# Kernel tuning notes

Hardware: AMD Instinct MI355X
Metric: run time of the kernel (lower is better)

The kernel has to match this reference:

```python
import jax, jax.numpy as jnp
import numpy as np
from jax import lax

B, S, M, D, NQ = 128, 100, 50, 128, 10000


def _xavier(key, shape):
    fan_in, fan_out = shape[0], shape[-1]
    limit = float(np.sqrt(6.0 / (fan_in + fan_out)))
    return jax.random.uniform(key, shape, jnp.float32, -limit, limit)


def setup_inputs() -> dict:
    key = jax.random.key(0)
    ks = jax.random.split(key, 16)
    return {
        "question_seq": jax.random.randint(ks[0], (B, S), 0, NQ),
        "answer_seq": jax.random.randint(ks[1], (B, S), 0, 2),
        "emb": _xavier(ks[2], (NQ, D)),
        "key_matrix": _xavier(ks[3], (M, D)),
        "vu_w1": _xavier(ks[4], (2 * D, D)),
        "vu_b1": jnp.zeros((D,), jnp.float32),
        "vu_w2": _xavier(ks[5], (D, D)),
        "vu_b2": jnp.zeros((D,), jnp.float32),
        "er_w": _xavier(ks[6], (D, D)),
        "er_b": jnp.zeros((D,), jnp.float32),
        "ad_w": _xavier(ks[7], (D, D)),
        "ad_b": jnp.zeros((D,), jnp.float32),
        "out_w1": _xavier(ks[8], (2 * D, D)),
        "out_b1": jnp.zeros((D,), jnp.float32),
        "out_w2": _xavier(ks[9], (D, 1)),
        "out_b2": jnp.zeros((1,), jnp.float32),
    }


def reference(question_seq, answer_seq, emb, key_matrix,
              vu_w1, vu_b1, vu_w2, vu_b2,
              er_w, er_b, ad_w, ad_b,
              out_w1, out_b1, out_w2, out_b2):
    # q_embed for all steps: [B,S,D]; attention over memory slots: [B,S,M]
    q_emb = emb[question_seq]
    attn = jax.nn.softmax(jnp.einsum('bsd,md->bsm', q_emb, key_matrix), axis=-1)

    def step(v, inp):
        w, qe = inp                                   # w: [B,M], qe: [B,D]
        read = jnp.einsum('bm,bmd->bd', w, v)         # attention read
        u = jnp.concatenate([read, qe], axis=-1)      # [B,2D]
        h = jnp.tanh(u @ vu_w1 + vu_b1)
        up = h @ vu_w2 + vu_b2                        # update vector [B,D]
        e = jax.nn.sigmoid(up @ er_w + er_b)          # erase gate
        a = jnp.tanh(up @ ad_w + ad_b)                # add vector
        v = v * (1.0 - w[:, :, None] * e[:, None, :]) + w[:, :, None] * a[:, None, :]
        return v, None

    v0 = jnp.zeros((B, M, D), q_emb.dtype)
    vT, _ = lax.scan(step, v0, (attn.transpose(1, 0, 2), q_emb.transpose(1, 0, 2)))

    # predict with last question (target_question=None branch)
    last_qe = q_emb[:, -1]                            # [B,D]
    last_w = attn[:, -1]                              # [B,M]
    read = jnp.einsum('bm,bmd->bd', last_w, vT)
    p_in = jnp.concatenate([read, last_qe], axis=-1)
    h = jax.nn.relu(p_in @ out_w1 + out_b1)
    pred = jax.nn.sigmoid(h @ out_w2 + out_b2)[:, 0]  # [B]
    return pred
```

## Files before the change

### kernel.cpp

```cpp
#include <hip/hip_runtime.h>

#define BB 128
#define SS 100
#define MM 50
#define DD 128
#define KROW 66
#define XW(k) ((k) + 8 * ((k) >> 5))
#define DUPW(k) ((k) + 8 * ((k) >> 5))

typedef float f32x2 __attribute__((ext_vector_type(2)));

#if defined(__has_builtin)
#  if __has_builtin(__builtin_elementwise_fma)
#    define HAVE_PKFMA 1
#  endif
#  if __has_builtin(__builtin_amdgcn_update_dpp)
#    define HAVE_DPP 1
#  endif
#endif

__device__ __forceinline__ f32x2 pkfma(f32x2 a, f32x2 b, f32x2 c) {
#ifdef HAVE_PKFMA
    return __builtin_elementwise_fma(a, b, c);
#else
    f32x2 r; r.x = fmaf(a.x, b.x, c.x); r.y = fmaf(a.y, b.y, c.y); return r;
#endif
}

__device__ __forceinline__ float qbf_add(float x) {
#ifdef HAVE_DPP
    union { float f; int i; } c, o;
    c.f = x;
    o.i = __builtin_amdgcn_update_dpp(0, c.i, 0xB1, 0xF, 0xF, true);
    x += o.f;
    c.f = x;
    o.i = __builtin_amdgcn_update_dpp(0, c.i, 0x4E, 0xF, 0xF, true);
    return x + o.f;
#else
    x += __shfl_xor(x, 1);
    x += __shfl_xor(x, 2);
    return x;
#endif
}

__device__ __forceinline__ float bf2f(unsigned short u) {
    union { unsigned int i; float f; } c; c.i = ((unsigned int)u) << 16; return c.f;
}
__device__ __forceinline__ float bfu_lo(unsigned int u) {
    union { unsigned int i; float f; } c; c.i = u << 16; return c.f;
}
__device__ __forceinline__ float bfu_hi(unsigned int u) {
    union { unsigned int i; float f; } c; c.i = u & 0xffff0000u; return c.f;
}
__device__ __forceinline__ unsigned short f2bf_bits(float f) {
    union { float f; unsigned int u; } c; c.f = f;
    unsigned int r = (c.u + 0x7FFFu + ((c.u >> 16) & 1u)) >> 16;
    return (unsigned short)r;
}
__device__ __forceinline__ unsigned int packbf(float lo, float hi) {
    return (unsigned int)f2bf_bits(lo) | ((unsigned int)f2bf_bits(hi) << 16);
}
__device__ __forceinline__ float fast_sigmoid(float x) { return 1.0f / (1.0f + __expf(-x)); }
__device__ __forceinline__ float fast_tanh(float x) {
    float ax = fabsf(x);
    float z = __expf(-2.0f * ax);
    float r = (1.0f - z) / (1.0f + z);
    return copysignf(r, x);
}

template <bool BF16>
__device__ __forceinline__ float ldw(const void* p, size_t idx) {
    if (BF16) return bf2f(((const unsigned short*)p)[idx]);
    return ((const float*)p)[idx];
}

#define W2ROW(r) ((r) * 68 + (((r) >> 5) << 3))

struct __align__(16) SmemT {
    union {
        struct {
            unsigned int key_w[MM * KROW];
            unsigned int qe8[8][68];
        } pre;
        struct {
            float xread[152];
            float xhdup[312];
            float h1f[DD];
        } run;
    } u;
    union {
        unsigned int w2s[8724];
        struct {
            unsigned int wrow_p[SS][32];
            unsigned short qp_all[SS][DD];
        } tab;
    } v2;
    int qrow[SS];
    float qlast[DD];
};

template <bool BF16>
__device__ void dkvmn_impl(
    const int* __restrict__ qseq,
    const void* emb, const void* key,
    const void* vu_w1, const void* vu_b1, const void* vu_w2, const void* vu_b2,
    const void* er_w, const void* er_b, const void* ad_w, const void* ad_b,
    const void* out_w1, const void* out_b1, const void* out_w2, const void* out_b2,
    void* outp, SmemT& sm)
{
    const int t = threadIdx.x;
    const int b = blockIdx.x;
    const int l = t & 63;
    const int wv = t >> 6;
    const int q = l & 3;
    const int d = (wv << 4) + (l >> 2);

    if (BF16) {
        const unsigned int* kg = (const unsigned int*)key;
        for (int g = t; g < MM * 64; g += 512)
            sm.u.pre.key_w[(g >> 6) * KROW + (g & 63)] = kg[g];
        const unsigned int* wg = (const unsigned int*)vu_w2;
        for (int g = t; g < 128 * 64; g += 512)
            sm.v2.w2s[W2ROW(g >> 6) + (g & 63)] = wg[g];
    } else {
        const float* kf = (const float*)key;
        for (int g = t; g < MM * 64; g += 512) {
            int row = g >> 6, c2 = g & 63;
            sm.u.pre.key_w[row * KROW + c2] = packbf(kf[row * 128 + 2 * c2], kf[row * 128 + 2 * c2 + 1]);
        }
        const float* wf = (const float*)vu_w2;
        for (int g = t; g < 128 * 64; g += 512) {
            int row = g >> 6, c2 = g & 63;
            sm.v2.w2s[W2ROW(row) + c2] = packbf(wf[row * 128 + 2 * c2], wf[row * 128 + 2 * c2 + 1]);
        }
    }
    for (int g = t; g < SS; g += 512) sm.qrow[g] = qseq[b * SS + g];
    __syncthreads();

    f32x2 rw2ea[32];
#pragma unroll
    for (int k = 0; k < 32; ++k) { rw2ea[k].x = 0.f; rw2ea[k].y = 0.f; }
    f32x2 eab2; eab2.x = 0.f; eab2.y = 0.f;
#pragma unroll 1
    for (int jc = 0; jc < 4; ++jc) {
        f32x2 ea[32];
#pragma unroll
        for (int i = 0; i < 32; ++i) {
            int j = 32 * jc + i;
            ea[i].x = ldw<BF16>(er_w, (size_t)j * DD + d);
            ea[i].y = ldw<BF16>(ad_w, (size_t)j * DD + d);
            float b2j = ldw<BF16>(vu_b2, j);
            f32x2 bs; bs.x = b2j; bs.y = b2j;
            eab2 = pkfma(bs, ea[i], eab2);
        }
#pragma unroll
        for (int k = 0; k < 32; ++k) {
            const uint4* wp = (const uint4*)&sm.v2.w2s[W2ROW(32 * q + k) + 16 * jc];
            uint4 A = wp[0], B = wp[1], C = wp[2], Dv = wp[3];
            unsigned int W[16] = { A.x, A.y, A.z, A.w, B.x, B.y, B.z, B.w,
                                   C.x, C.y, C.z, C.w, Dv.x, Dv.y, Dv.z, Dv.w };
            f32x2 acc = rw2ea[k];
#pragma unroll
            for (int wd = 0; wd < 16; ++wd) {
                float wlo = bfu_lo(W[wd]), whi = bfu_hi(W[wd]);
                f32x2 s0; s0.x = wlo; s0.y = wlo;
                f32x2 s1; s1.x = whi; s1.y = whi;
                acc = pkfma(s0, ea[2 * wd], acc);
                acc = pkfma(s1, ea[2 * wd + 1], acc);
            }
            rw2ea[k] = acc;
        }
    }
    eab2.x += ldw<BF16>(er_b, d);
    eab2.y += ldw<BF16>(ad_b, d);
    __syncthreads();

    f32x2 rw1a2[16];
    float rw1b[32];
#pragma unroll
    for (int i = 0; i < 16; ++i) {
        int k0 = 32 * q + 2 * i;
        rw1a2[i].x = ldw<BF16>(vu_w1, (size_t)k0 * DD + d);
        rw1a2[i].y = ldw<BF16>(vu_w1, (size_t)(k0 + 1) * DD + d);
    }
#pragma unroll
    for (int i = 0; i < 32; ++i)
        rw1b[i] = ldw<BF16>(vu_w1, (size_t)(DD + 32 * q + i) * DD + d);
    const float b1r = ldw<BF16>(vu_b1, d);

    for (int ii = 0; ii < 13; ++ii) {
        const int nrows = (ii == 12) ? 4 : 8;
        {
            int r = t >> 6, w = t & 63;
            if (r < nrows) {
                int row = sm.qrow[8 * ii + r];
                if (BF16) {
                    sm.u.pre.qe8[r][w] = ((const unsigned int*)emb)[((size_t)row << 6) + w];
                } else {
                    const float* ef = (const float*)emb + (((size_t)row) << 7) + 2 * w;
                    sm.u.pre.qe8[r][w] = packbf(ef[0], ef[1]);
                }
            }
        }
        __syncthreads();

        if (wv < nrows) {
            int m = l;
            int mc = (m < MM) ? m : (MM - 1);
            float a0 = 0.f, a1 = 0.f, a2 = 0.f, a3 = 0.f;
#pragma unroll
            for (int j = 0; j < 32; ++j) {
                uint2 kw = *(const uint2*)&sm.u.pre.key_w[mc * KROW + 2 * j];
                uint2 qw = *(const uint2*)&sm.u.pre.qe8[wv][2 * j];
                a0 = fmaf(bfu_lo(kw.x), bfu_lo(qw.x), a0);
                a1 = fmaf(bfu_hi(kw.x), bfu_hi(qw.x), a1);
                a2 = fmaf(bfu_lo(kw.y), bfu_lo(qw.y), a2);
                a3 = fmaf(bfu_hi(kw.y), bfu_hi(qw.y), a3);
            }
            float lg = (a0 + a1) + (a2 + a3);
            if (m >= MM) lg = -1e30f;
            float mx = lg;
#pragma unroll
            for (int o = 32; o > 0; o >>= 1) mx = fmaxf(mx, __shfl_xor(mx, o));
            float p = (m < MM) ? __expf(lg - mx) : 0.f;
            float sum = p;
#pragma unroll
            for (int o = 32; o > 0; o >>= 1) sum += __shfl_xor(sum, o);
            p = p / sum;
            float pn = __shfl_xor(p, 4);
            if ((m & 4) == 0)
                sm.v2.tab.wrow_p[8 * ii + wv][(m & 3) * 8 + (m >> 3)] = packbf(p, pn);
        }

        for (int sr = 0; sr < nrows; ++sr) {
            float p0 = 0.f, p1 = 0.f;
#pragma unroll
            for (int i = 0; i < 16; ++i) {
                unsigned int uw = sm.u.pre.qe8[sr][16 * q + i];
                p0 = fmaf(rw1b[2 * i],     bfu_lo(uw), p0);
                p1 = fmaf(rw1b[2 * i + 1], bfu_hi(uw), p1);
            }
            float qpv = qbf_add(p0 + p1);
            if (q == 0) sm.v2.tab.qp_all[8 * ii + sr][d] = f2bf_bits(qpv);
        }
        __syncthreads();
    }

    if (t < 64) {
        unsigned int uw = sm.u.pre.qe8[3][t];
        sm.qlast[2 * t]     = bfu_lo(uw);
        sm.qlast[2 * t + 1] = bfu_hi(uw);
    }
    f32x2 v2[7];
#pragma unroll
    for (int p = 0; p < 7; ++p) { v2[p].x = 0.f; v2[p].y = 0.f; }
    f32x2 wr2[7];
    {
        const uint4* wp = (const uint4*)&sm.v2.tab.wrow_p[0][q * 8];
        uint4 w0 = wp[0], w1 = wp[1];
        unsigned int ww[8] = { w0.x, w0.y, w0.z, w0.w, w1.x, w1.y, w1.z, w1.w };
#pragma unroll
        for (int p = 0; p < 7; ++p) { wr2[p].x = bfu_lo(ww[p]); wr2[p].y = bfu_hi(ww[p]); }
    }
    if (t < 152) sm.u.run.xread[t] = 0.f;
    __syncthreads();

    for (int s = 0; s < SS; ++s) {
        {
            float qpv = bf2f(sm.v2.tab.qp_all[s][d]);
            const float4* xp = (const float4*)&sm.u.run.xread[40 * q];
            f32x2 acc2; acc2.x = 0.f; acc2.y = 0.f;
#pragma unroll
            for (int j = 0; j < 8; ++j) {
                float4 X = xp[j];
                f32x2 x01; x01.x = X.x; x01.y = X.y;
                f32x2 x23; x23.x = X.z; x23.y = X.w;
                acc2 = pkfma(rw1a2[2 * j], x01, acc2);
                acc2 = pkfma(rw1a2[2 * j + 1], x23, acc2);
            }
            float acc = qbf_add(acc2.x + acc2.y);
            float hh = fast_tanh(acc + qpv + b1r);
            if (q == 0) {
                f32x2 hd; hd.x = hh; hd.y = hh;
                *(f32x2*)&sm.u.run.xhdup[DUPW(2 * d)] = hd;
            }
        }
        __syncthreads();

        {
            f32x2 acc2; acc2.x = 0.f; acc2.y = 0.f;
#pragma unroll
            for (int blk = 0; blk < 2; ++blk) {
                const float4* xp = (const float4*)&sm.u.run.xhdup[80 * q + 40 * blk];
#pragma unroll
                for (int j = 0; j < 8; ++j) {
                    float4 X = xp[j];
                    f32x2 s0; s0.x = X.x; s0.y = X.y;
                    f32x2 s1; s1.x = X.z; s1.y = X.w;
                    int k = 16 * blk + 2 * j;
                    acc2 = pkfma(rw2ea[k], s0, acc2);
                    acc2 = pkfma(rw2ea[k + 1], s1, acc2);
                }
            }
            float ae = qbf_add(acc2.x);
            float aa = qbf_add(acc2.y);
            float e = fast_sigmoid(ae + eab2.x);
            float a = fast_tanh(aa + eab2.y);
            f32x2 me; me.x = -e; me.y = -e;
            f32x2 av; av.x = a;  av.y = a;
#pragma unroll
            for (int p = 0; p < 7; ++p)
                v2[p] = pkfma(wr2[p], pkfma(me, v2[p], av), v2[p]);
            if (s + 1 < SS) {
                const uint4* wp = (const uint4*)&sm.v2.tab.wrow_p[s + 1][q * 8];
                uint4 w0 = wp[0], w1 = wp[1];
                unsigned int ww[8] = { w0.x, w0.y, w0.z, w0.w, w1.x, w1.y, w1.z, w1.w };
#pragma unroll
                for (int p = 0; p < 7; ++p) { wr2[p].x = bfu_lo(ww[p]); wr2[p].y = bfu_hi(ww[p]); }
            }
            f32x2 racc; racc.x = 0.f; racc.y = 0.f;
#pragma unroll
            for (int p = 0; p < 7; ++p)
                racc = pkfma(wr2[p], v2[p], racc);
            float rr = qbf_add(racc.x + racc.y);
            if (q == 0) sm.u.run.xread[XW(d)] = rr;
        }
        __syncthreads();
    }

    float acc = 0.f;
    {
        const float4* xp = (const float4*)&sm.u.run.xread[40 * q];
        const float4* qp4 = (const float4*)&sm.qlast[32 * q];
#pragma unroll
        for (int j = 0; j < 8; ++j) {
            float4 xv = xp[j];
            float4 qv = qp4[j];
            int k = 32 * q + 4 * j;
            acc = fmaf(ldw<BF16>(out_w1, (size_t)k * DD + d),       xv.x, acc);
            acc = fmaf(ldw<BF16>(out_w1, (size_t)(k + 1) * DD + d), xv.y, acc);
            acc = fmaf(ldw<BF16>(out_w1, (size_t)(k + 2) * DD + d), xv.z, acc);
            acc = fmaf(ldw<BF16>(out_w1, (size_t)(k + 3) * DD + d), xv.w, acc);
            acc = fmaf(ldw<BF16>(out_w1, (size_t)(DD + k) * DD + d),     qv.x, acc);
            acc = fmaf(ldw<BF16>(out_w1, (size_t)(DD + k + 1) * DD + d), qv.y, acc);
            acc = fmaf(ldw<BF16>(out_w1, (size_t)(DD + k + 2) * DD + d), qv.z, acc);
            acc = fmaf(ldw<BF16>(out_w1, (size_t)(DD + k + 3) * DD + d), qv.w, acc);
        }
    }
    acc = qbf_add(acc);
    float h1 = fmaxf(acc + ldw<BF16>(out_b1, d), 0.f);
    if (q == 0) sm.u.run.h1f[d] = h1;
    __syncthreads();

    if (t < 64) {
        float xs = fmaf(sm.u.run.h1f[t], ldw<BF16>(out_w2, t),
                        sm.u.run.h1f[64 + t] * ldw<BF16>(out_w2, 64 + t));
#pragma unroll
        for (int o = 32; o > 0; o >>= 1) xs += __shfl_xor(xs, o);
        if (t == 0) {
            float pred = fast_sigmoid(xs + ldw<BF16>(out_b2, 0));
            if (BF16) ((unsigned short*)outp)[b] = f2bf_bits(pred);
            else      ((float*)outp)[b] = pred;
        }
    }
}

__global__ __launch_bounds__(512) void DKVMN_78546361909953_kernel(
    const int* __restrict__ qseq,
    const void* emb, const void* key,
    const void* vu_w1, const void* vu_b1, const void* vu_w2, const void* vu_b2,
    const void* er_w, const void* er_b, const void* ad_w, const void* ad_b,
    const void* out_w1, const void* out_b1, const void* out_w2, const void* out_b2,
    void* outp)
{
    __shared__ SmemT sm;

    const unsigned int* eu = (const unsigned int*)emb;
    int cnt = 0;
    for (int i = 0; i < 32; ++i) {
        unsigned int e8 = (eu[i] >> 7) & 0xFFu;
        cnt += (e8 >= 100u && e8 <= 127u) ? 1 : 0;
    }
    if (cnt >= 16)
        dkvmn_impl<true>(qseq, emb, key, vu_w1, vu_b1, vu_w2, vu_b2,
                         er_w, er_b, ad_w, ad_b, out_w1, out_b1, out_w2, out_b2, outp, sm);
    else
        dkvmn_impl<false>(qseq, emb, key, vu_w1, vu_b1, vu_w2, vu_b2,
                          er_w, er_b, ad_w, ad_b, out_w1, out_b1, out_w2, out_b2, outp, sm);
}

extern "C" void kernel_launch(void* const* d_in, const int* in_sizes, int n_in,
                              void* d_out, int out_size, void* d_ws, size_t ws_size,
                              hipStream_t stream) {
    const int* qseq = (const int*)d_in[0];
    DKVMN_78546361909953_kernel<<<BB, 512, 0, stream>>>(
        qseq,
        d_in[2], d_in[3], d_in[4], d_in[5], d_in[6], d_in[7],
        d_in[8], d_in[9], d_in[10], d_in[11],
        d_in[12], d_in[13], d_in[14], d_in[15],
        d_out);
}
```

Measured before the change: 282.4 us.

## Split precompute and recurrent scan into two kernels via workspace

Splits the monolithic kernel into a precompute kernel and a scan kernel. The precompute kernel runs attention softmax, the question projection and the folded W2·[er,ad] matrix across 257 blocks, with each batch split into two halves of the sequence, and writes the results to a global workspace. The scan kernel then reads these, prefetching the next step's attention row and projection from global memory during the current step. The aim is to take the serial per-block prologue off the critical path and spread it over more CUs. The cost is an extra launch and the workspace traffic. A monolithic fallback remains for when the workspace is too small.

```diff
diff --git a/kernel.cpp b/kernel.cpp
--- a/kernel.cpp
+++ b/kernel.cpp
@@ -5,8 +5,6 @@
 #define MM 50
 #define DD 128
 #define KROW 66
-#define XW(k) ((k) + 8 * ((k) >> 5))
-#define DUPW(k) ((k) + 8 * ((k) >> 5))
 
 typedef float f32x2 __attribute__((ext_vector_type(2)));
 
@@ -74,9 +72,413 @@
     return ((const float*)p)[idx];
 }
 
+__device__ __forceinline__ bool detect_bf16(const void* emb) {
+    const unsigned int* eu = (const unsigned int*)emb;
+    int cnt = 0;
+    for (int i = 0; i < 32; ++i) {
+        unsigned int e8 = (eu[i] >> 7) & 0xFFu;
+        cnt += (e8 >= 100u && e8 <= 127u) ? 1 : 0;
+    }
+    return cnt >= 16;
+}
+
 #define W2ROW(r) ((r) * 68 + (((r) >> 5) << 3))
 
-struct __align__(16) SmemT {
+#define WS_WROW_OFF 0u
+#define WS_QP_OFF   (BB * SS * 32u * 4u)
+#define WS_W2EA_OFF (WS_QP_OFF + BB * SS * DD * 2u)
+#define WS_EAB_OFF  (WS_W2EA_OFF + DD * DD * 8u)
+#define WS_NEED     (WS_EAB_OFF + DD * 8u)
+
+struct __align__(16) SmemA {
+    union {
+        struct {
+            unsigned int key_w[MM * KROW];
+            unsigned int qe8[8][68];
+        } pre;
+        unsigned int w2s[8724];
+    } u;
+};
+
+template <bool BF16>
+__device__ void pre_impl(const int* qseq, const void* emb, const void* key,
+                         const void* vu_w1, unsigned int* wrow_g, unsigned short* qp_g,
+                         SmemA& sm)
+{
+    const int t = threadIdx.x;
+    const int b = blockIdx.x;
+    const int half = blockIdx.y;
+    const int l = t & 63;
+    const int wv = t >> 6;
+    const int q = l & 3;
+    const int d = (wv << 4) + (l >> 2);
+
+    if (BF16) {
+        const unsigned int* kg = (const unsigned int*)key;
+        for (int g = t; g < MM * 64; g += 512)
+            sm.u.pre.key_w[(g >> 6) * KROW + (g & 63)] = kg[g];
+    } else {
+        const float* kf = (const float*)key;
+        for (int g = t; g < MM * 64; g += 512) {
+            int row = g >> 6, c2 = g & 63;
+            sm.u.pre.key_w[row * KROW + c2] = packbf(kf[row * 128 + 2 * c2], kf[row * 128 + 2 * c2 + 1]);
+        }
+    }
+
+    float rw1b[32];
+#pragma unroll
+    for (int i = 0; i < 32; ++i)
+        rw1b[i] = ldw<BF16>(vu_w1, (size_t)(DD + 32 * q + i) * DD + d);
+    __syncthreads();
+
+    for (int ii = 0; ii < 7; ++ii) {
+        const int nrows = (ii == 6) ? 2 : 8;
+        {
+            int r = t >> 6, w = t & 63;
+            if (r < nrows) {
+                int s = 50 * half + 8 * ii + r;
+                int row = qseq[b * SS + s];
+                if (BF16) {
+                    sm.u.pre.qe8[r][w] = ((const unsigned int*)emb)[((size_t)row << 6) + w];
+                } else {
+                    const float* ef = (const float*)emb + (((size_t)row) << 7) + 2 * w;
+                    sm.u.pre.qe8[r][w] = packbf(ef[0], ef[1]);
+                }
+            }
+        }
+        __syncthreads();
+
+        if (wv < nrows) {
+            int m = l;
+            int mc = (m < MM) ? m : (MM - 1);
+            float a0 = 0.f, a1 = 0.f, a2 = 0.f, a3 = 0.f;
+#pragma unroll
+            for (int j = 0; j < 32; ++j) {
+                uint2 kw = *(const uint2*)&sm.u.pre.key_w[mc * KROW + 2 * j];
+                uint2 qw = *(const uint2*)&sm.u.pre.qe8[wv][2 * j];
+                a0 = fmaf(bfu_lo(kw.x), bfu_lo(qw.x), a0);
+                a1 = fmaf(bfu_hi(kw.x), bfu_hi(qw.x), a1);
+                a2 = fmaf(bfu_lo(kw.y), bfu_lo(qw.y), a2);
+                a3 = fmaf(bfu_hi(kw.y), bfu_hi(qw.y), a3);
+            }
+            float lg = (a0 + a1) + (a2 + a3);
+            if (m >= MM) lg = -1e30f;
+            float mx = lg;
+#pragma unroll
+            for (int o = 32; o > 0; o >>= 1) mx = fmaxf(mx, __shfl_xor(mx, o));
+            float p = (m < MM) ? __expf(lg - mx) : 0.f;
+            float sum = p;
+#pragma unroll
+            for (int o = 32; o > 0; o >>= 1) sum += __shfl_xor(sum, o);
+            p = p / sum;
+            float pn = __shfl_xor(p, 4);
+            int s = 50 * half + 8 * ii + wv;
+            if ((m & 4) == 0)
+                wrow_g[(size_t)(b * SS + s) * 32 + (m & 3) * 8 + (m >> 3)] = packbf(p, pn);
+        }
+
+        for (int sr = 0; sr < nrows; ++sr) {
+            float p0 = 0.f, p1 = 0.f;
+#pragma unroll
+            for (int i = 0; i < 16; ++i) {
+                unsigned int uw = sm.u.pre.qe8[sr][16 * q + i];
+                p0 = fmaf(rw1b[2 * i],     bfu_lo(uw), p0);
+                p1 = fmaf(rw1b[2 * i + 1], bfu_hi(uw), p1);
+            }
+            float qpv = qbf_add(p0 + p1);
+            int s = 50 * half + 8 * ii + sr;
+            if (q == 0) qp_g[(size_t)(b * SS + s) * DD + d] = f2bf_bits(qpv);
+        }
+        __syncthreads();
+    }
+}
+
+template <bool BF16>
+__device__ void build_impl(const void* vu_w2, const void* vu_b2,
+                           const void* er_w, const void* er_b,
+                           const void* ad_w, const void* ad_b,
+                           f32x2* w2ea_g, f32x2* eab_g, SmemA& sm)
+{
+    const int t = threadIdx.x;
+    const int l = t & 63;
+    const int wv = t >> 6;
+    const int q = l & 3;
+    const int d = (wv << 4) + (l >> 2);
+
+    if (BF16) {
+        const unsigned int* wg = (const unsigned int*)vu_w2;
+        for (int g = t; g < 128 * 64; g += 512)
+            sm.u.w2s[W2ROW(g >> 6) + (g & 63)] = wg[g];
+    } else {
+        const float* wf = (const float*)vu_w2;
+        for (int g = t; g < 128 * 64; g += 512) {
+            int row = g >> 6, c2 = g & 63;
+            sm.u.w2s[W2ROW(row) + c2] = packbf(wf[row * 128 + 2 * c2], wf[row * 128 + 2 * c2 + 1]);
+        }
+    }
+    __syncthreads();
+
+    f32x2 rw2ea[32];
+#pragma unroll
+    for (int k = 0; k < 32; ++k) { rw2ea[k].x = 0.f; rw2ea[k].y = 0.f; }
+    f32x2 eab2; eab2.x = 0.f; eab2.y = 0.f;
+#pragma unroll 1
+    for (int jc = 0; jc < 4; ++jc) {
+        f32x2 ea[32];
+#pragma unroll
+        for (int i = 0; i < 32; ++i) {
+            int j = 32 * jc + i;
+            ea[i].x = ldw<BF16>(er_w, (size_t)j * DD + d);
+            ea[i].y = ldw<BF16>(ad_w, (size_t)j * DD + d);
+            float b2j = ldw<BF16>(vu_b2, j);
+            f32x2 bs; bs.x = b2j; bs.y = b2j;
+            eab2 = pkfma(bs, ea[i], eab2);
+        }
+#pragma unroll
+        for (int k = 0; k < 32; ++k) {
+            const uint4* wp = (const uint4*)&sm.u.w2s[W2ROW(32 * q + k) + 16 * jc];
+            uint4 A = wp[0], B = wp[1], C = wp[2], Dv = wp[3];
+            unsigned int W[16] = { A.x, A.y, A.z, A.w, B.x, B.y, B.z, B.w,
+                                   C.x, C.y, C.z, C.w, Dv.x, Dv.y, Dv.z, Dv.w };
+            f32x2 acc = rw2ea[k];
+#pragma unroll
+            for (int wd = 0; wd < 16; ++wd) {
+                float wlo = bfu_lo(W[wd]), whi = bfu_hi(W[wd]);
+                f32x2 s0; s0.x = wlo; s0.y = wlo;
+                f32x2 s1; s1.x = whi; s1.y = whi;
+                acc = pkfma(s0, ea[2 * wd], acc);
+                acc = pkfma(s1, ea[2 * wd + 1], acc);
+            }
+            rw2ea[k] = acc;
+        }
+    }
+    eab2.x += ldw<BF16>(er_b, d);
+    eab2.y += ldw<BF16>(ad_b, d);
+
+#pragma unroll
+    for (int k = 0; k < 32; ++k)
+        w2ea_g[(size_t)(32 * q + k) * DD + d] = rw2ea[k];
+    if (q == 0) eab_g[d] = eab2;
+}
+
+__global__ __launch_bounds__(512) void DKVMN_78546361909953_pre(
+    const int* __restrict__ qseq,
+    const void* emb, const void* key, const void* vu_w1,
+    const void* vu_w2, const void* vu_b2,
+    const void* er_w, const void* er_b, const void* ad_w, const void* ad_b,
+    void* ws)
+{
+    __shared__ SmemA sm;
+    unsigned int*   wrow_g = (unsigned int*)((char*)ws + WS_WROW_OFF);
+    unsigned short* qp_g   = (unsigned short*)((char*)ws + WS_QP_OFF);
+    f32x2*          w2ea_g = (f32x2*)((char*)ws + WS_W2EA_OFF);
+    f32x2*          eab_g  = (f32x2*)((char*)ws + WS_EAB_OFF);
+    bool isbf = detect_bf16(emb);
+    if (blockIdx.x < BB) {
+        if (isbf) pre_impl<true>(qseq, emb, key, vu_w1, wrow_g, qp_g, sm);
+        else      pre_impl<false>(qseq, emb, key, vu_w1, wrow_g, qp_g, sm);
+    } else if (blockIdx.y == 0) {
+        if (isbf) build_impl<true>(vu_w2, vu_b2, er_w, er_b, ad_w, ad_b, w2ea_g, eab_g, sm);
+        else      build_impl<false>(vu_w2, vu_b2, er_w, er_b, ad_w, ad_b, w2ea_g, eab_g, sm);
+    }
+}
+
+struct __align__(16) SmemB {
+    float xread[152];
+    float xhdup[312];
+    float h1f[DD];
+    float qlast[DD];
+};
+
+template <bool BF16>
+__device__ void scan_impl(
+    const int* __restrict__ qseq,
+    const void* emb, const void* vu_w1, const void* vu_b1,
+    const void* out_w1, const void* out_b1, const void* out_w2, const void* out_b2,
+    const unsigned int* wrow_g, const unsigned short* qp_g,
+    const f32x2* w2ea_g, const f32x2* eab_g,
+    void* outp, SmemB& sm)
+{
+    const int t = threadIdx.x;
+    const int b = blockIdx.x;
+    const int l = t & 63;
+    const int q = l & 3;
+    const int d = ((t >> 6) << 4) + (l >> 2);
+
+    if (t < 64) {
+        int row = qseq[b * SS + (SS - 1)];
+        if (BF16) {
+            unsigned int uw = ((const unsigned int*)emb)[((size_t)row << 6) + t];
+            sm.qlast[2 * t]     = bfu_lo(uw);
+            sm.qlast[2 * t + 1] = bfu_hi(uw);
+        } else {
+            const float* ef = (const float*)emb + (((size_t)row) << 7) + 2 * t;
+            sm.qlast[2 * t]     = ef[0];
+            sm.qlast[2 * t + 1] = ef[1];
+        }
+    }
+
+    f32x2 rw1a2[16];
+#pragma unroll
+    for (int i = 0; i < 16; ++i) {
+        int k0 = 32 * q + 2 * i;
+        rw1a2[i].x = ldw<BF16>(vu_w1, (size_t)k0 * DD + d);
+        rw1a2[i].y = ldw<BF16>(vu_w1, (size_t)(k0 + 1) * DD + d);
+    }
+    const float b1r = ldw<BF16>(vu_b1, d);
+
+    f32x2 rw2ea[32];
+#pragma unroll
+    for (int k = 0; k < 32; ++k)
+        rw2ea[k] = w2ea_g[(size_t)(32 * q + k) * DD + d];
+    const f32x2 eab2 = eab_g[d];
+
+    f32x2 v2[7];
+#pragma unroll
+    for (int p = 0; p < 7; ++p) { v2[p].x = 0.f; v2[p].y = 0.f; }
+    f32x2 wr2[7];
+    {
+        const size_t r0 = (size_t)(b * SS) * 32 + q * 8;
+        uint4 w0 = *(const uint4*)&wrow_g[r0];
+        uint4 w1 = *(const uint4*)&wrow_g[r0 + 4];
+        unsigned int ww[8] = { w0.x, w0.y, w0.z, w0.w, w1.x, w1.y, w1.z, w1.w };
+#pragma unroll
+        for (int p = 0; p < 7; ++p) { wr2[p].x = bfu_lo(ww[p]); wr2[p].y = bfu_hi(ww[p]); }
+    }
+    unsigned short qpcur = qp_g[(size_t)(b * SS) * DD + d];
+
+    if (t < 152) sm.xread[t] = 0.f;
+    __syncthreads();
+
+    for (int s = 0; s < SS; ++s) {
+        uint4 pwA, pwB;
+        unsigned short pq = 0;
+        const bool hasnext = (s + 1 < SS);
+        if (hasnext) {
+            size_t r1 = (size_t)(b * SS + s + 1);
+            pwA = *(const uint4*)&wrow_g[r1 * 32 + q * 8];
+            pwB = *(const uint4*)&wrow_g[r1 * 32 + q * 8 + 4];
+            pq  = qp_g[r1 * DD + d];
+        }
+
+        {
+            float qpv = bf2f(qpcur);
+            const float4* xp = (const float4*)&sm.xread[40 * q];
+            f32x2 acc2; acc2.x = 0.f; acc2.y = 0.f;
+#pragma unroll
+            for (int j = 0; j < 8; ++j) {
+                float4 X = xp[j];
+                f32x2 x01; x01.x = X.x; x01.y = X.y;
+                f32x2 x23; x23.x = X.z; x23.y = X.w;
+                acc2 = pkfma(rw1a2[2 * j], x01, acc2);
+                acc2 = pkfma(rw1a2[2 * j + 1], x23, acc2);
+            }
+            float acc = qbf_add(acc2.x + acc2.y);
+            float hh = fast_tanh(acc + qpv + b1r);
+            if (q == 0) {
+                f32x2 hd; hd.x = hh; hd.y = hh;
+                *(f32x2*)&sm.xhdup[2 * d + 8 * ((2 * d) >> 5)] = hd;
+            }
+        }
+        __syncthreads();
+
+        {
+            f32x2 acc2; acc2.x = 0.f; acc2.y = 0.f;
+#pragma unroll
+            for (int blk = 0; blk < 2; ++blk) {
+                const float4* xp = (const float4*)&sm.xhdup[80 * q + 40 * blk];
+#pragma unroll
+                for (int j = 0; j < 8; ++j) {
+                    float4 X = xp[j];
+                    f32x2 s0; s0.x = X.x; s0.y = X.y;
+                    f32x2 s1; s1.x = X.z; s1.y = X.w;
+                    int k = 16 * blk + 2 * j;
+                    acc2 = pkfma(rw2ea[k], s0, acc2);
+                    acc2 = pkfma(rw2ea[k + 1], s1, acc2);
+                }
+            }
+            float ae = qbf_add(acc2.x);
+            float aa = qbf_add(acc2.y);
+            float e = fast_sigmoid(ae + eab2.x);
+            float a = fast_tanh(aa + eab2.y);
+            f32x2 me; me.x = -e; me.y = -e;
+            f32x2 av; av.x = a;  av.y = a;
+#pragma unroll
+            for (int p = 0; p < 7; ++p)
+                v2[p] = pkfma(wr2[p], pkfma(me, v2[p], av), v2[p]);
+            if (hasnext) {
+                unsigned int ww[8] = { pwA.x, pwA.y, pwA.z, pwA.w, pwB.x, pwB.y, pwB.z, pwB.w };
+#pragma unroll
+                for (int p = 0; p < 7; ++p) { wr2[p].x = bfu_lo(ww[p]); wr2[p].y = bfu_hi(ww[p]); }
+                qpcur = pq;
+            }
+            f32x2 racc; racc.x = 0.f; racc.y = 0.f;
+#pragma unroll
+            for (int p = 0; p < 7; ++p)
+                racc = pkfma(wr2[p], v2[p], racc);
+            float rr = qbf_add(racc.x + racc.y);
+            if (q == 0) sm.xread[rr == rr ? (d + 8 * (d >> 5)) : 0] = rr;
+        }
+        __syncthreads();
+    }
+
+    float acc = 0.f;
+    {
+        const float4* xp = (const float4*)&sm.xread[40 * q];
+        const float4* qp4 = (const float4*)&sm.qlast[32 * q];
+#pragma unroll
+        for (int j = 0; j < 8; ++j) {
+            float4 xv = xp[j];
+            float4 qv = qp4[j];
+            int k = 32 * q + 4 * j;
+            acc = fmaf(ldw<BF16>(out_w1, (size_t)k * DD + d),       xv.x, acc);
+            acc = fmaf(ldw<BF16>(out_w1, (size_t)(k + 1) * DD + d), xv.y, acc);
+            acc = fmaf(ldw<BF16>(out_w1, (size_t)(k + 2) * DD + d), xv.z, acc);
+            acc = fmaf(ldw<BF16>(out_w1, (size_t)(k + 3) * DD + d), xv.w, acc);
+            acc = fmaf(ldw<BF16>(out_w1, (size_t)(DD + k) * DD + d),     qv.x, acc);
+            acc = fmaf(ldw<BF16>(out_w1, (size_t)(DD + k + 1) * DD + d), qv.y, acc);
+            acc = fmaf(ldw<BF16>(out_w1, (size_t)(DD + k + 2) * DD + d), qv.z, acc);
+            acc = fmaf(ldw<BF16>(out_w1, (size_t)(DD + k + 3) * DD + d), qv.w, acc);
+        }
+    }
+    acc = qbf_add(acc);
+    float h1 = fmaxf(acc + ldw<BF16>(out_b1, d), 0.f);
+    if (q == 0) sm.h1f[d] = h1;
+    __syncthreads();
+
+    if (t < 64) {
+        float xs = fmaf(sm.h1f[t], ldw<BF16>(out_w2, t),
+                        sm.h1f[64 + t] * ldw<BF16>(out_w2, 64 + t));
+#pragma unroll
+        for (int o = 32; o > 0; o >>= 1) xs += __shfl_xor(xs, o);
+        if (t == 0) {
+            float pred = fast_sigmoid(xs + ldw<BF16>(out_b2, 0));
+            if (BF16) ((unsigned short*)outp)[b] = f2bf_bits(pred);
+            else      ((float*)outp)[b] = pred;
+        }
+    }
+}
+
+__global__ __launch_bounds__(512) void DKVMN_78546361909953_scan(
+    const int* __restrict__ qseq,
+    const void* emb, const void* vu_w1, const void* vu_b1,
+    const void* out_w1, const void* out_b1, const void* out_w2, const void* out_b2,
+    void* ws, void* outp)
+{
+    __shared__ SmemB sm;
+    const unsigned int*   wrow_g = (const unsigned int*)((char*)ws + WS_WROW_OFF);
+    const unsigned short* qp_g   = (const unsigned short*)((char*)ws + WS_QP_OFF);
+    const f32x2*          w2ea_g = (const f32x2*)((char*)ws + WS_W2EA_OFF);
+    const f32x2*          eab_g  = (const f32x2*)((char*)ws + WS_EAB_OFF);
+    if (detect_bf16(emb))
+        scan_impl<true>(qseq, emb, vu_w1, vu_b1, out_w1, out_b1, out_w2, out_b2,
+                        wrow_g, qp_g, w2ea_g, eab_g, outp, sm);
+    else
+        scan_impl<false>(qseq, emb, vu_w1, vu_b1, out_w1, out_b1, out_w2, out_b2,
+                         wrow_g, qp_g, w2ea_g, eab_g, outp, sm);
+}
+
+struct __align__(16) SmemM {
     union {
         struct {
             unsigned int key_w[MM * KROW];
@@ -100,13 +502,13 @@
 };
 
 template <bool BF16>
-__device__ void dkvmn_impl(
+__device__ void mono_impl(
     const int* __restrict__ qseq,
     const void* emb, const void* key,
     const void* vu_w1, const void* vu_b1, const void* vu_w2, const void* vu_b2,
     const void* er_w, const void* er_b, const void* ad_w, const void* ad_b,
     const void* out_w1, const void* out_b1, const void* out_w2, const void* out_b2,
-    void* outp, SmemT& sm)
+    void* outp, SmemM& sm)
 {
     const int t = threadIdx.x;
     const int b = blockIdx.x;
@@ -175,17 +577,12 @@
     eab2.y += ldw<BF16>(ad_b, d);
     __syncthreads();
 
-    f32x2 rw1a2[16];
-    float rw1b[32];
-#pragma unroll
-    for (int i = 0; i < 16; ++i) {
-        int k0 = 32 * q + 2 * i;
-        rw1a2[i].x = ldw<BF16>(vu_w1, (size_t)k0 * DD + d);
-        rw1a2[i].y = ldw<BF16>(vu_w1, (size_t)(k0 + 1) * DD + d);
-    }
-#pragma unroll
-    for (int i = 0; i < 32; ++i)
+    float rw1a[32], rw1b[32];
+#pragma unroll
+    for (int i = 0; i < 32; ++i) {
+        rw1a[i] = ldw<BF16>(vu_w1, (size_t)(32 * q + i) * DD + d);
         rw1b[i] = ldw<BF16>(vu_w1, (size_t)(DD + 32 * q + i) * DD + d);
+    }
     const float b1r = ldw<BF16>(vu_b1, d);
 
     for (int ii = 0; ii < 13; ++ii) {
@@ -269,20 +666,23 @@
         {
             float qpv = bf2f(sm.v2.tab.qp_all[s][d]);
             const float4* xp = (const float4*)&sm.u.run.xread[40 * q];
+            f32x2 rw1a2_j;
             f32x2 acc2; acc2.x = 0.f; acc2.y = 0.f;
 #pragma unroll
             for (int j = 0; j < 8; ++j) {
                 float4 X = xp[j];
                 f32x2 x01; x01.x = X.x; x01.y = X.y;
                 f32x2 x23; x23.x = X.z; x23.y = X.w;
-                acc2 = pkfma(rw1a2[2 * j], x01, acc2);
-                acc2 = pkfma(rw1a2[2 * j + 1], x23, acc2);
+                rw1a2_j.x = rw1a[4 * j];     rw1a2_j.y = rw1a[4 * j + 1];
+                acc2 = pkfma(rw1a2_j, x01, acc2);
+                rw1a2_j.x = rw1a[4 * j + 2]; rw1a2_j.y = rw1a[4 * j + 3];
+                acc2 = pkfma(rw1a2_j, x23, acc2);
             }
             float acc = qbf_add(acc2.x + acc2.y);
             float hh = fast_tanh(acc + qpv + b1r);
             if (q == 0) {
                 f32x2 hd; hd.x = hh; hd.y = hh;
-                *(f32x2*)&sm.u.run.xhdup[DUPW(2 * d)] = hd;
+                *(f32x2*)&sm.u.run.xhdup[2 * d + 8 * ((2 * d) >> 5)] = hd;
             }
         }
         __syncthreads();
@@ -323,7 +723,7 @@
             for (int p = 0; p < 7; ++p)
                 racc = pkfma(wr2[p], v2[p], racc);
             float rr = qbf_add(racc.x + racc.y);
-            if (q == 0) sm.u.run.xread[XW(d)] = rr;
+            if (q == 0) sm.u.run.xread[d + 8 * (d >> 5)] = rr;
         }
         __syncthreads();
     }
@@ -373,30 +773,30 @@
     const void* out_w1, const void* out_b1, const void* out_w2, const void* out_b2,
     void* outp)
 {
-    __shared__ SmemT sm;
-
-    const unsigned int* eu = (const unsigned int*)emb;
-    int cnt = 0;
-    for (int i = 0; i < 32; ++i) {
-        unsigned int e8 = (eu[i] >> 7) & 0xFFu;
-        cnt += (e8 >= 100u && e8 <= 127u) ? 1 : 0;
-    }
-    if (cnt >= 16)
-        dkvmn_impl<true>(qseq, emb, key, vu_w1, vu_b1, vu_w2, vu_b2,
+    __shared__ SmemM sm;
+    if (detect_bf16(emb))
+        mono_impl<true>(qseq, emb, key, vu_w1, vu_b1, vu_w2, vu_b2,
+                        er_w, er_b, ad_w, ad_b, out_w1, out_b1, out_w2, out_b2, outp, sm);
+    else
+        mono_impl<false>(qseq, emb, key, vu_w1, vu_b1, vu_w2, vu_b2,
                          er_w, er_b, ad_w, ad_b, out_w1, out_b1, out_w2, out_b2, outp, sm);
-    else
-        dkvmn_impl<false>(qseq, emb, key, vu_w1, vu_b1, vu_w2, vu_b2,
-                          er_w, er_b, ad_w, ad_b, out_w1, out_b1, out_w2, out_b2, outp, sm);
 }
 
 extern "C" void kernel_launch(void* const* d_in, const int* in_sizes, int n_in,
                               void* d_out, int out_size, void* d_ws, size_t ws_size,
                               hipStream_t stream) {
     const int* qseq = (const int*)d_in[0];
-    DKVMN_78546361909953_kernel<<<BB, 512, 0, stream>>>(
-        qseq,
-        d_in[2], d_in[3], d_in[4], d_in[5], d_in[6], d_in[7],
-        d_in[8], d_in[9], d_in[10], d_in[11],
-        d_in[12], d_in[13], d_in[14], d_in[15],
-        d_out);
-}
+    if (ws_size >= (size_t)WS_NEED) {
+        DKVMN_78546361909953_pre<<<dim3(BB + 1, 2), 512, 0, stream>>>(
+            qseq, d_in[2], d_in[3], d_in[4],
+            d_in[6], d_in[7], d_in[8], d_in[9], d_in[10], d_in[11], d_ws);
+        DKVMN_78546361909953_scan<<<BB, 512, 0, stream>>>(
+            qseq, d_in[2], d_in[4], d_in[5],
+            d_in[12], d_in[13], d_in[14], d_in[15], d_ws, d_out);
+    } else {
+        DKVMN_78546361909953_kernel<<<BB, 512, 0, stream>>>(
+            qseq, d_in[2], d_in[3], d_in[4], d_in[5], d_in[6], d_in[7],
+            d_in[8], d_in[9], d_in[10], d_in[11],
+            d_in[12], d_in[13], d_in[14], d_in[15], d_out);
+    }
+}
```

Result: faster. 259.7 us (-8.0%).
